# Optimization experiments

Hardware: AMD Instinct MI355X
Metric: run time of the kernel (lower is better)

The kernel has to match this reference:

```python
import jax, jax.numpy as jnp
import numpy as np

N = 65536      # total nodes = 64 graphs x 1024 nodes
B = 64         # graphs in batch
NPG = 1024     # nodes per graph
EPG = 16384    # edges per graph (avg degree 16)
H = 4          # attention heads
D = 32         # per-head out feats (graph_hiddens = [32, 32])
IN_DIM = 128
NEG_SLOPE = 0.2

def _glorot(key, shape):
    return jax.random.normal(key, shape, jnp.float32) / jnp.sqrt(jnp.float32(shape[0]))

def setup_inputs() -> dict:
    key = jax.random.key(0)
    ks = jax.random.split(key, 16)
    x = jax.random.normal(ks[0], (N, IN_DIM), jnp.float32)
    # edges generated within each graph: endpoint = graph_offset + local index
    offs = (jnp.arange(B, dtype=jnp.int32) * NPG)[:, None]
    src = (jax.random.randint(ks[1], (B, EPG), 0, NPG, jnp.int32) + offs).reshape(-1)
    dst = (jax.random.randint(ks[2], (B, EPG), 0, NPG, jnp.int32) + offs).reshape(-1)
    gid = jnp.repeat(jnp.arange(B, dtype=jnp.int32), NPG)
    return {
        "x": x, "src": src, "dst": dst, "gid": gid,
        # GATv2 layer 1 (in 128 -> H*D)
        "Ws1": _glorot(ks[3], (IN_DIM, H * D)), "bs1": jnp.zeros((H * D,), jnp.float32),
        "Wd1": _glorot(ks[4], (IN_DIM, H * D)), "bd1": jnp.zeros((H * D,), jnp.float32),
        "attn1": jax.random.normal(ks[5], (H, D), jnp.float32) * 0.1,
        # GATv2 layer 2 (in 32 -> H*D)
        "Ws2": _glorot(ks[6], (D, H * D)), "bs2": jnp.zeros((H * D,), jnp.float32),
        "Wd2": _glorot(ks[7], (D, H * D)), "bd2": jnp.zeros((H * D,), jnp.float32),
        "attn2": jax.random.normal(ks[8], (H, D), jnp.float32) * 0.1,
        # global attention pooling gate Linear(D, 1)
        "gW": _glorot(ks[9], (D, 1)), "gb": jnp.zeros((1,), jnp.float32),
    }

def gatv2_maxpool(h, src, dst, Ws, bs, Wd, bd, attn):
    """DGL GATv2Conv (share_weights=False, attn_drop=0/eval) + MaxPool1d over heads."""
    fs = (h @ Ws + bs).reshape(N, H, D)   # fc_src
    fd = (h @ Wd + bd).reshape(N, H, D)   # fc_dst
    e = jax.nn.leaky_relu(fs[src] + fd[dst], NEG_SLOPE)     # [E,H,D]
    s = jnp.einsum('ehd,hd->eh', e, attn)                    # per-edge logits [E,H]
    m = jax.lax.stop_gradient(jax.ops.segment_max(s, dst, num_segments=N))
    a = jnp.exp(s - m[dst])
    z = jax.ops.segment_sum(a, dst, num_segments=N)
    alpha = a / z[dst]                                       # edge softmax per dst node
    out = jax.ops.segment_sum(alpha[:, :, None] * fs[src], dst, num_segments=N)  # [N,H,D]
    return out.max(axis=1)                                   # maxpool over heads -> [N,D]

def reference(x, src, dst, gid, Ws1, bs1, Wd1, bd1, attn1, Ws2, bs2, Wd2, bd2, attn2, gW, gb):
    h = gatv2_maxpool(x, src, dst, Ws1, bs1, Wd1, bd1, attn1)
    h = gatv2_maxpool(h, src, dst, Ws2, bs2, Wd2, bd2, attn2)
    # GlobalAttentionPooling: softmax(gate) over nodes within each graph
    g = (h @ gW + gb)[:, 0]                                  # [N]
    gm = jax.lax.stop_gradient(jax.ops.segment_max(g, gid, num_segments=B))
    ga = jnp.exp(g - gm[gid])
    gz = jax.ops.segment_sum(ga, gid, num_segments=B)
    w = ga / gz[gid]
    return jax.ops.segment_sum(w[:, None] * h, gid, num_segments=B)  # [B,D]
```

## Files before the change

kernel.cpp:

```cpp
#include <hip/hip_runtime.h>
#include <hip/hip_fp16.h>
#include <math.h>

#define N_NODES 65536
#define B_GRAPHS 64
#define NPG 1024
#define EPG 16384
#define E_TOTAL (B_GRAPHS * EPG)
#define NEG 0.2f

typedef float f32x4 __attribute__((ext_vector_type(4)));
typedef _Float16 f16x8 __attribute__((ext_vector_type(8)));
typedef _Float16 h2v __attribute__((ext_vector_type(2)));
typedef int i32x4 __attribute__((ext_vector_type(4)));
typedef unsigned int uint32;
typedef unsigned short u16;

union FragH { i32x4 i; f16x8 h; uint32 u[4]; };
union H2U { uint32 u; h2v h; };

__device__ __forceinline__ float fast_exp2(float x) {
    float r;
    asm("v_exp_f32 %0, %1" : "=v"(r) : "v"(x));
    return r;
}

__device__ __forceinline__ uint32 f2h2(float a, float b) {
    __half2 h = __float22half2_rn(make_float2(a, b));
    return *(uint32*)&h;
}

__device__ __forceinline__ void fma_mix_lo(float& acc, float p, uint32 fv) {
    asm("v_fma_mix_f32 %0, %1, %2, %0 op_sel_hi:[0,1,0]" : "+v"(acc) : "v"(p), "v"(fv));
}
__device__ __forceinline__ void fma_mix_hi(float& acc, float p, uint32 fv) {
    asm("v_fma_mix_f32 %0, %1, %2, %0 op_sel:[0,1,0] op_sel_hi:[0,1,0]" : "+v"(acc) : "v"(p), "v"(fv));
}

__device__ __forceinline__ float dot_term(uint32 fvu, h2v fdv, h2v neg2, h2v av, float accum) {
    H2U fv; fv.u = fvu;
    h2v e = fv.h + fdv;
    h2v en = e * neg2;
    h2v em;
    asm("v_pk_max_f16 %0, %1, %2" : "=v"(em) : "v"(e), "v"(en));
    float sp;
    asm("v_dot2_f32_f16 %0, %1, %2, %3" : "=v"(sp) : "v"(em), "v"(av), "v"(accum));
    return sp;
}

__global__ __launch_bounds__(1024) void k_prep(const int* __restrict__ src, const int* __restrict__ dst,
                                               int* __restrict__ rowptr, int* __restrict__ col,
                                               const float* __restrict__ Ws1, const float* __restrict__ Wd1,
                                               const float* __restrict__ Ws2, const float* __restrict__ Wd2,
                                               __half* __restrict__ Wf1, __half* __restrict__ Wf2) {
    __shared__ int cnt[NPG];
    __shared__ int tmp[NPG];
    __shared__ int scol[EPG];
    if (blockIdx.x >= B_GRAPHS) {
        int id = (blockIdx.x - B_GRAPHS) * 1024 + threadIdx.x;
        if (id < 32768) {
            int j = id & 7, l = (id >> 3) & 63, c = (id >> 9) & 3, T = id >> 11;
            int k = c * 32 + (l >> 4) * 8 + j;
            int n = (T & 7) * 16 + (l & 15);
            const float* W = (T < 8) ? Ws1 : Wd1;
            Wf1[id] = __float2half_rn(W[k * 128 + n]);
        } else if (id < 40960) {
            int rem = id - 32768;
            int j = rem & 7, l = (rem >> 3) & 63, T = rem >> 9;
            int k = (l >> 4) * 8 + j;
            int n = (T & 7) * 16 + (l & 15);
            const float* W = (T < 8) ? Ws2 : Wd2;
            Wf2[rem] = __float2half_rn(W[k * 128 + n]);
        }
        return;
    }
    int g = blockIdx.x, tid = threadIdx.x;
    int ebase = g * EPG;
    cnt[tid] = 0;
    __syncthreads();
    for (int e = tid; e < EPG; e += 1024)
        atomicAdd(&cnt[dst[ebase + e] & (NPG - 1)], 1);
    __syncthreads();
    int* a = cnt; int* b = tmp;
#pragma unroll
    for (int off = 1; off < 1024; off <<= 1) {
        int u = a[tid] + ((tid >= off) ? a[tid - off] : 0);
        __syncthreads();
        b[tid] = u;
        __syncthreads();
        int* t = a; a = b; b = t;
    }
    int excl = tid ? a[tid - 1] : 0;
    rowptr[g * NPG + tid] = ebase + excl;
    if (g == B_GRAPHS - 1 && tid == 0) rowptr[N_NODES] = E_TOTAL;
    b[tid] = excl;
    __syncthreads();
    for (int e = tid; e < EPG; e += 1024) {
        int d = dst[ebase + e] & (NPG - 1);
        int p = atomicAdd(&b[d], 1);
        scol[p] = src[ebase + e];
    }
    __syncthreads();
    int4* cg = (int4*)(col + ebase);
    const int4* cs = (const int4*)scol;
    for (int i = tid; i < EPG / 4; i += 1024) cg[i] = cs[i];
}

template <int K>
__global__ __launch_bounds__(512) void k_gemm_mfma(const float* __restrict__ X,
                                                   const __half* __restrict__ Wf,
                                                   const float* __restrict__ bs, const float* __restrict__ bd,
                                                   u16* __restrict__ fsd) {
    constexpr int NC = K / 32;
    constexpr int LDK = K + 8;
    __shared__ float xsbuf[4352];
    float* xs = xsbuf;
    u16* eb = (u16*)xsbuf;
    int tid = threadIdx.x;
    int lane = tid & 63, wv = tid >> 6;
    int l15 = lane & 15, kg = lane >> 4;
    int ng = wv & 1, Tb = (wv >> 1) * 4;
    int nb = blockIdx.x * 32;

    if (K == 128) {
#pragma unroll
        for (int j = 0; j < 2; ++j) {
            int f = tid + j * 512;
            int r = f >> 5, c4 = f & 31;
            *(float4*)(xs + r * LDK + c4 * 4) = *(const float4*)(X + (size_t)(nb + r) * K + c4 * 4);
        }
    } else {
        if (tid < 256) {
            int r = tid >> 3, c4 = tid & 7;
            *(float4*)(xs + r * LDK + c4 * 4) = *(const float4*)(X + (size_t)(nb + r) * K + c4 * 4);
        }
    }
    __syncthreads();

    int ridx = ng * 16 + l15;
    FragH xf[NC];
#pragma unroll
    for (int c = 0; c < NC; ++c) {
        const float* xr = xs + ridx * LDK + c * 32 + kg * 8;
        float4 v0 = *(const float4*)xr;
        float4 v1 = *(const float4*)(xr + 4);
        xf[c].u[0] = f2h2(v0.x, v0.y);
        xf[c].u[1] = f2h2(v0.z, v0.w);
        xf[c].u[2] = f2h2(v1.x, v1.y);
        xf[c].u[3] = f2h2(v1.z, v1.w);
    }

    f32x4 acc[4];
#pragma unroll
    for (int i = 0; i < 4; ++i) acc[i] = (f32x4){0.f, 0.f, 0.f, 0.f};

#pragma unroll
    for (int i = 0; i < 4; ++i) {
        int T = Tb + i;
        const __half* wp = Wf + ((size_t)(T * NC) * 64 + lane) * 8;
#pragma unroll
        for (int c = 0; c < NC; ++c) {
            FragH wfr;
            wfr.i = *(const i32x4*)(wp + (size_t)c * 512);
            acc[i] = __builtin_amdgcn_mfma_f32_16x16x32_f16(wfr.h, xf[c].h, acc[i], 0, 0, 0);
        }
    }
    __syncthreads();

#pragma unroll
    for (int i = 0; i < 4; ++i) {
        int T = Tb + i;
        const float* bp = (T < 8) ? bs : bd;
        float4 bv = *(const float4*)(bp + (T & 7) * 16 + kg * 4);
        uint2 pk;
        pk.x = f2h2(acc[i][0] + bv.x, acc[i][1] + bv.y);
        pk.y = f2h2(acc[i][2] + bv.z, acc[i][3] + bv.w);
        int colh = (T & 7) * 16 + (T >> 3) * 128 + kg * 4;
        *(uint2*)(eb + (ng * 16 + l15) * 264 + colh) = pk;
    }
    __syncthreads();

#pragma unroll
    for (int j = 0; j < 2; ++j) {
        int f = tid + j * 512;
        int r = f >> 5, c = f & 31;
        i32x4 v = *(const i32x4*)(eb + r * 264 + c * 8);
        *(i32x4*)(fsd + (size_t)(nb + r) * 256 + c * 8) = v;
    }
}

__global__ __launch_bounds__(256) void k_edge(const u16* __restrict__ fsd,
                                              const int* __restrict__ rowptr, const int* __restrict__ col,
                                              const float* __restrict__ attn, float* __restrict__ hout) {
    int w = threadIdx.x >> 6, lane = threadIdx.x & 63;
    int bid = blockIdx.x;
    int nb = (bid & 7) * 512 + (bid >> 3);
    int q = lane >> 4, s = lane & 15;
    int n = nb * 16 + w * 4 + q;
    const char* fsdb = (const char*)fsd;

    const float* ap = attn + (s >> 2) * 32 + (s & 3) * 8;
    float4 a0 = *(const float4*)ap;
    float4 a1 = *(const float4*)(ap + 4);
    const float L2E = 1.44269504089f;
    h2v av0, av1, av2, av3;
    { H2U t; t.u = f2h2(a0.x * L2E, a0.y * L2E); av0 = t.h;
      t.u = f2h2(a0.z * L2E, a0.w * L2E); av1 = t.h;
      t.u = f2h2(a1.x * L2E, a1.y * L2E); av2 = t.h;
      t.u = f2h2(a1.z * L2E, a1.w * L2E); av3 = t.h; }
    h2v neg2; neg2[0] = (_Float16)NEG; neg2[1] = (_Float16)NEG;

    i32x4 fdq = *(const i32x4*)(fsdb + ((size_t)n << 9) + 256 + (s << 4));
    H2U fd0, fd1, fd2, fd3;
    fd0.u = (uint32)fdq[0]; fd1.u = (uint32)fdq[1]; fd2.u = (uint32)fdq[2]; fd3.u = (uint32)fdq[3];

    int start = rowptr[n];
    int end   = rowptr[n + 1];
    int deg = end - start;
    int m = deg;
    { int t16 = __shfl_xor(m, 16); m = (t16 > m) ? t16 : m;
      int t32 = __shfl_xor(m, 32); m = (t32 > m) ? t32 : m; }
    int niter = (__builtin_amdgcn_readfirstlane(m) + 3) >> 2;

    uint32 soff = (uint32)(s << 4);

    auto colat = [&](int e) -> uint32 {
        int idxc = (e < deg) ? (start + e) : 0;
        return (uint32)col[idxc];
    };
    auto gather = [&](uint32 cval) -> i32x4 {
        uint32 cc = cval & (N_NODES - 1);
        return *(const i32x4*)(fsdb + (((size_t)cc << 9) | soff));
    };

    float z = 0.f;
    float c0 = 0.f, c1 = 0.f, c2 = 0.f, c3 = 0.f, c4 = 0.f, c5 = 0.f, c6 = 0.f, c7 = 0.f;

    auto proc = [&](i32x4 f, int e) {
        uint32 w0 = (uint32)f[0], w1 = (uint32)f[1], w2 = (uint32)f[2], w3 = (uint32)f[3];
        float sp = dot_term(w0, fd0.h, neg2, av0, 0.f);
        sp = dot_term(w1, fd1.h, neg2, av1, sp);
        sp = dot_term(w2, fd2.h, neg2, av2, sp);
        sp = dot_term(w3, fd3.h, neg2, av3, sp);
        sp += __shfl_xor(sp, 1);
        sp += __shfl_xor(sp, 2);
        float pe = fast_exp2(sp);
        pe = (e < deg) ? pe : 0.f;
        z += pe;
        fma_mix_lo(c0, pe, w0); fma_mix_hi(c1, pe, w0);
        fma_mix_lo(c2, pe, w1); fma_mix_hi(c3, pe, w1);
        fma_mix_lo(c4, pe, w2); fma_mix_hi(c5, pe, w2);
        fma_mix_lo(c6, pe, w3); fma_mix_hi(c7, pe, w3);
    };

    uint32 cnxt0 = colat(4), cnxt1 = colat(5), cnxt2 = colat(6), cnxt3 = colat(7);
    i32x4 fv0 = gather(colat(0)), fv1 = gather(colat(1)), fv2 = gather(colat(2)), fv3 = gather(colat(3));

    for (int k = 0; k < niter; ++k) {
        int e = k * 4;
        i32x4 a = fv0, b = fv1, c = fv2, d = fv3;
        fv0 = gather(cnxt0); fv1 = gather(cnxt1); fv2 = gather(cnxt2); fv3 = gather(cnxt3);
        cnxt0 = colat(e + 8); cnxt1 = colat(e + 9); cnxt2 = colat(e + 10); cnxt3 = colat(e + 11);
        proc(a, e + 0);
        proc(b, e + 1);
        proc(c, e + 2);
        proc(d, e + 3);
    }

    float r = (z > 0.f) ? 1.f / z : 0.f;
    c0 *= r; c1 *= r; c2 *= r; c3 *= r; c4 *= r; c5 *= r; c6 *= r; c7 *= r;

    c0 = fmaxf(c0, __shfl_xor(c0, 4)); c0 = fmaxf(c0, __shfl_xor(c0, 8));
    c1 = fmaxf(c1, __shfl_xor(c1, 4)); c1 = fmaxf(c1, __shfl_xor(c1, 8));
    c2 = fmaxf(c2, __shfl_xor(c2, 4)); c2 = fmaxf(c2, __shfl_xor(c2, 8));
    c3 = fmaxf(c3, __shfl_xor(c3, 4)); c3 = fmaxf(c3, __shfl_xor(c3, 8));
    c4 = fmaxf(c4, __shfl_xor(c4, 4)); c4 = fmaxf(c4, __shfl_xor(c4, 8));
    c5 = fmaxf(c5, __shfl_xor(c5, 4)); c5 = fmaxf(c5, __shfl_xor(c5, 8));
    c6 = fmaxf(c6, __shfl_xor(c6, 4)); c6 = fmaxf(c6, __shfl_xor(c6, 8));
    c7 = fmaxf(c7, __shfl_xor(c7, 4)); c7 = fmaxf(c7, __shfl_xor(c7, 8));

    if (s < 4) {
        float* op = hout + ((size_t)n << 5) + (s << 3);
        *(float4*)op = make_float4(c0, c1, c2, c3);
        *(float4*)(op + 4) = make_float4(c4, c5, c6, c7);
    }
}

__global__ __launch_bounds__(256) void k_pool(const float* __restrict__ h2, const float* __restrict__ gW,
                                              const float* __restrict__ gb, float* __restrict__ out) {
    int b = blockIdx.x, tid = threadIdx.x;
    __shared__ float ga[NPG];
    __shared__ float red[256];
    __shared__ float gws[32];
    const float* hb = h2 + (size_t)b * NPG * 32;
    if (tid < 32) gws[tid] = gW[tid];
    __syncthreads();
    float gbv = gb[0];
    float lmax = -INFINITY;
    float gloc[4];
#pragma unroll
    for (int j = 0; j < 4; ++j) {
        int nl = tid + j * 256;
        const float* row = hb + nl * 32;
        float dot = 0.f;
#pragma unroll
        for (int c = 0; c < 32; c += 4) {
            float4 v = *(const float4*)(row + c);
            dot += v.x * gws[c] + v.y * gws[c + 1] + v.z * gws[c + 2] + v.w * gws[c + 3];
        }
        gloc[j] = dot + gbv;
        lmax = fmaxf(lmax, gloc[j]);
    }
    red[tid] = lmax; __syncthreads();
    for (int s2 = 128; s2 > 0; s2 >>= 1) { if (tid < s2) red[tid] = fmaxf(red[tid], red[tid + s2]); __syncthreads(); }
    float m = red[0];
    __syncthreads();
    float lsum = 0.f;
#pragma unroll
    for (int j = 0; j < 4; ++j) {
        int nl = tid + j * 256;
        float a = __expf(gloc[j] - m);
        ga[nl] = a;
        lsum += a;
    }
    red[tid] = lsum; __syncthreads();
    for (int s2 = 128; s2 > 0; s2 >>= 1) { if (tid < s2) red[tid] += red[tid + s2]; __syncthreads(); }
    float z = red[0];
    __syncthreads();
    int d = tid & 31, ng = tid >> 5;
    float acc = 0.f;
    for (int nl = ng; nl < NPG; nl += 8) acc += ga[nl] * hb[nl * 32 + d];
    red[tid] = acc; __syncthreads();
    if (tid < 32) {
        float s = red[tid];
#pragma unroll
        for (int g2 = 1; g2 < 8; ++g2) s += red[g2 * 32 + tid];
        out[b * 32 + tid] = s / z;
    }
}

extern "C" void kernel_launch(void* const* d_in, const int* in_sizes, int n_in,
                              void* d_out, int out_size, void* d_ws, size_t ws_size,
                              hipStream_t stream) {
    const float* x     = (const float*)d_in[0];
    const int*   src   = (const int*)d_in[1];
    const int*   dst   = (const int*)d_in[2];
    const float* Ws1   = (const float*)d_in[4];
    const float* bs1   = (const float*)d_in[5];
    const float* Wd1   = (const float*)d_in[6];
    const float* bd1   = (const float*)d_in[7];
    const float* attn1 = (const float*)d_in[8];
    const float* Ws2   = (const float*)d_in[9];
    const float* bs2   = (const float*)d_in[10];
    const float* Wd2   = (const float*)d_in[11];
    const float* bd2   = (const float*)d_in[12];
    const float* attn2 = (const float*)d_in[13];
    const float* gW    = (const float*)d_in[14];
    const float* gb    = (const float*)d_in[15];
    float* out = (float*)d_out;

    u16* fsd   = (u16*)d_ws;
    float* h1  = (float*)(fsd + (size_t)N_NODES * 256);
    float* h2  = h1 + (size_t)N_NODES * 32;
    int* rowptr = (int*)(h2 + (size_t)N_NODES * 32);
    int* col    = rowptr + (N_NODES + 4);
    __half* Wf1 = (__half*)(col + E_TOTAL);
    __half* Wf2 = Wf1 + 32768;

    k_prep<<<B_GRAPHS + 40, 1024, 0, stream>>>(src, dst, rowptr, col,
                                               Ws1, Wd1, Ws2, Wd2, Wf1, Wf2);

    k_gemm_mfma<128><<<N_NODES / 32, 512, 0, stream>>>(x, Wf1, bs1, bd1, fsd);
    k_edge<<<N_NODES / 16, 256, 0, stream>>>(fsd, rowptr, col, attn1, h1);

    k_gemm_mfma<32><<<N_NODES / 32, 512, 0, stream>>>(h1, Wf2, bs2, bd2, fsd);
    k_edge<<<N_NODES / 16, 256, 0, stream>>>(fsd, rowptr, col, attn2, h2);

    k_pool<<<B_GRAPHS, 256, 0, stream>>>(h2, gW, gb, out);
}
```

Measured before the change: 143.5 us.

## Sort destination nodes by degree per graph to balance wavefront edge loops

During CSR construction, k_prep now builds a per-graph histogram of in-degrees (capped at 63) and writes a permutation that groups nodes of similar degree. k_edge handles nodes in that permuted order, so the four nodes in a wavefront have similar degrees and the max-degree loop count wastes fewer lanes. The column array also stores the source index pre-shifted by 9, which removes a mask and shift from each gather address. The cost is an extra perm array, another histogram pass in prep, and an indirect node lookup per lane. Output rows are now written in scattered order within each graph.

```diff
diff --git a/kernel.cpp b/kernel.cpp
--- a/kernel.cpp
+++ b/kernel.cpp
@@ -49,13 +49,17 @@
 }
 
 __global__ __launch_bounds__(1024) void k_prep(const int* __restrict__ src, const int* __restrict__ dst,
-                                               int* __restrict__ rowptr, int* __restrict__ col,
+                                               int* __restrict__ rowptr, int* __restrict__ colb,
+                                               int* __restrict__ perm,
                                                const float* __restrict__ Ws1, const float* __restrict__ Wd1,
                                                const float* __restrict__ Ws2, const float* __restrict__ Wd2,
                                                __half* __restrict__ Wf1, __half* __restrict__ Wf2) {
     __shared__ int cnt[NPG];
     __shared__ int tmp[NPG];
+    __shared__ int degs[NPG];
     __shared__ int scol[EPG];
+    __shared__ int hd[64];
+    __shared__ int hcur[64];
     if (blockIdx.x >= B_GRAPHS) {
         int id = (blockIdx.x - B_GRAPHS) * 1024 + threadIdx.x;
         if (id < 32768) {
@@ -81,6 +85,7 @@
     for (int e = tid; e < EPG; e += 1024)
         atomicAdd(&cnt[dst[ebase + e] & (NPG - 1)], 1);
     __syncthreads();
+    degs[tid] = cnt[tid];
     int* a = cnt; int* b = tmp;
 #pragma unroll
     for (int off = 1; off < 1024; off <<= 1) {
@@ -98,12 +103,24 @@
     for (int e = tid; e < EPG; e += 1024) {
         int d = dst[ebase + e] & (NPG - 1);
         int p = atomicAdd(&b[d], 1);
-        scol[p] = src[ebase + e];
-    }
-    __syncthreads();
-    int4* cg = (int4*)(col + ebase);
+        scol[p] = src[ebase + e] << 9;
+    }
+    if (tid < 64) hd[tid] = 0;
+    __syncthreads();
+    int dc = degs[tid]; dc = (dc > 63) ? 63 : dc;
+    atomicAdd(&hd[dc], 1);
+    int4* cg = (int4*)(colb + ebase);
     const int4* cs = (const int4*)scol;
     for (int i = tid; i < EPG / 4; i += 1024) cg[i] = cs[i];
+    __syncthreads();
+    if (tid == 0) {
+        int run = 0;
+#pragma unroll 8
+        for (int i = 0; i < 64; ++i) { hcur[i] = run; run += hd[i]; }
+    }
+    __syncthreads();
+    int pos = atomicAdd(&hcur[dc], 1);
+    perm[g * NPG + pos] = g * NPG + tid;
 }
 
 template <int K>
@@ -190,13 +207,14 @@
 }
 
 __global__ __launch_bounds__(256) void k_edge(const u16* __restrict__ fsd,
-                                              const int* __restrict__ rowptr, const int* __restrict__ col,
+                                              const int* __restrict__ rowptr, const int* __restrict__ colb,
+                                              const int* __restrict__ perm,
                                               const float* __restrict__ attn, float* __restrict__ hout) {
     int w = threadIdx.x >> 6, lane = threadIdx.x & 63;
     int bid = blockIdx.x;
     int nb = (bid & 7) * 512 + (bid >> 3);
     int q = lane >> 4, s = lane & 15;
-    int n = nb * 16 + w * 4 + q;
+    int n = perm[nb * 16 + w * 4 + q];
     const char* fsdb = (const char*)fsd;
 
     const float* ap = attn + (s >> 2) * 32 + (s & 3) * 8;
@@ -226,11 +244,10 @@
 
     auto colat = [&](int e) -> uint32 {
         int idxc = (e < deg) ? (start + e) : 0;
-        return (uint32)col[idxc];
+        return (uint32)colb[idxc];
     };
     auto gather = [&](uint32 cval) -> i32x4 {
-        uint32 cc = cval & (N_NODES - 1);
-        return *(const i32x4*)(fsdb + (((size_t)cc << 9) | soff));
+        return *(const i32x4*)(fsdb + ((size_t)(cval | soff)));
     };
 
     float z = 0.f;
@@ -363,18 +380,19 @@
     float* h1  = (float*)(fsd + (size_t)N_NODES * 256);
     float* h2  = h1 + (size_t)N_NODES * 32;
     int* rowptr = (int*)(h2 + (size_t)N_NODES * 32);
-    int* col    = rowptr + (N_NODES + 4);
-    __half* Wf1 = (__half*)(col + E_TOTAL);
+    int* colb   = rowptr + (N_NODES + 4);
+    __half* Wf1 = (__half*)(colb + E_TOTAL);
     __half* Wf2 = Wf1 + 32768;
-
-    k_prep<<<B_GRAPHS + 40, 1024, 0, stream>>>(src, dst, rowptr, col,
+    int* perm   = (int*)(Wf2 + 8192);
+
+    k_prep<<<B_GRAPHS + 40, 1024, 0, stream>>>(src, dst, rowptr, colb, perm,
                                                Ws1, Wd1, Ws2, Wd2, Wf1, Wf2);
 
     k_gemm_mfma<128><<<N_NODES / 32, 512, 0, stream>>>(x, Wf1, bs1, bd1, fsd);
-    k_edge<<<N_NODES / 16, 256, 0, stream>>>(fsd, rowptr, col, attn1, h1);
+    k_edge<<<N_NODES / 16, 256, 0, stream>>>(fsd, rowptr, colb, perm, attn1, h1);
 
     k_gemm_mfma<32><<<N_NODES / 32, 512, 0, stream>>>(h1, Wf2, bs2, bd2, fsd);
-    k_edge<<<N_NODES / 16, 256, 0, stream>>>(fsd, rowptr, col, attn2, h2);
+    k_edge<<<N_NODES / 16, 256, 0, stream>>>(fsd, rowptr, colb, perm, attn2, h2);
 
     k_pool<<<B_GRAPHS, 256, 0, stream>>>(h2, gW, gb, out);
 }
```

Result: faster. 139.8 us (-2.6%).
